# Optimization experiments

Measured on AMD Instinct MI355X. Metric: run time of the kernel, lower is better.

The kernel has to match this reference:

```python
import jax, jax.numpy as jnp
import numpy as np
from jax import lax

B = 16384
NWIRES = 4


def _conv(x, w, b):
    # NCHW conv, stride 1, SAME padding (pad 1 for k=3)
    y = lax.conv_general_dilated(x, w, (1, 1), ((1, 1), (1, 1)),
                                 dimension_numbers=("NCHW", "OIHW", "NCHW"))
    return y + b[None, :, None, None]


def _pool2(x):
    b, c, h, w = x.shape
    return x.reshape(b, c, h // 2, 2, w // 2, 2).max(axis=(3, 5))


def _apply_1q(state, U, wire):
    # state: (B,2,2,2,2) complex; U: (B,2,2) complex
    s = jnp.moveaxis(state, wire + 1, -1)
    s = jnp.einsum("bij,b...j->b...i", U, s)
    return jnp.moveaxis(s, -1, wire + 1)


def _apply_cnot(state, c, t):
    s0 = jnp.take(state, 0, axis=c + 1)
    s1 = jnp.take(state, 1, axis=c + 1)
    ta = t + 1 if t < c else t  # target axis index after removing control axis
    s1 = jnp.flip(s1, axis=ta)
    return jnp.stack([s0, s1], axis=c + 1)


def _ry(th):
    c = jnp.cos(th / 2)
    s = jnp.sin(th / 2)
    U = jnp.stack([jnp.stack([c, -s], -1), jnp.stack([s, c], -1)], -2)
    return U.astype(jnp.complex64)


def _rz(th):
    e = jnp.exp(-0.5j * th.astype(jnp.complex64))
    z = jnp.zeros_like(e)
    return jnp.stack([jnp.stack([e, z], -1), jnp.stack([z, jnp.conj(e)], -1)], -2)


def _rx(th):
    c = jnp.cos(th / 2).astype(jnp.complex64)
    s = jnp.sin(th / 2).astype(jnp.complex64)
    return jnp.stack([jnp.stack([c, -1j * s], -1), jnp.stack([-1j * s, c], -1)], -2)


def _circuit(params):
    # params: (B, 16) -> PauliZ expvals (B, 4)
    b = params.shape[0]
    state = jnp.zeros((b, 16), jnp.complex64).at[:, 0].set(1.0).reshape(b, 2, 2, 2, 2)
    for i in range(NWIRES):
        state = _apply_1q(state, _ry(params[:, 4 * i + 0]), i)
        state = _apply_1q(state, _rz(params[:, 4 * i + 1]), i)
        state = _apply_1q(state, _rx(params[:, 4 * i + 2]), i)
        state = _apply_cnot(state, i, (i + 1) % NWIRES)
    probs = state.real ** 2 + state.imag ** 2  # (B,2,2,2,2)
    zs = []
    for i in range(NWIRES):
        p = probs.sum(axis=tuple(a for a in range(1, 5) if a != i + 1))  # (B,2)
        zs.append(p[:, 0] - p[:, 1])
    return jnp.stack(zs, axis=-1)


def setup_inputs() -> dict:
    key = jax.random.key(0)
    ks = jax.random.split(key, 12)
    d = {}
    d["x"] = jax.random.normal(ks[0], (B, 1, 28, 28), jnp.float32)
    d["conv1_w"] = jax.random.normal(ks[1], (4, 1, 3, 3), jnp.float32) * 0.3
    d["conv1_b"] = jax.random.normal(ks[2], (4,), jnp.float32) * 0.1
    d["conv2_w"] = jax.random.normal(ks[3], (4, 4, 3, 3), jnp.float32) * 0.15
    d["conv2_b"] = jax.random.normal(ks[4], (4,), jnp.float32) * 0.1
    d["pl_w"] = jax.random.normal(ks[5], (16, 196), jnp.float32) * 0.07
    d["pl_b"] = jax.random.normal(ks[6], (16,), jnp.float32) * 0.05
    d["ro_w"] = jax.random.normal(ks[7], (4, 4), jnp.float32) * 0.5
    d["ro_b"] = jax.random.normal(ks[8], (4,), jnp.float32) * 0.1
    d["bn_w"] = jnp.ones((4,), jnp.float32)
    d["bn_b"] = jnp.zeros((4,), jnp.float32)
    return d


def reference(x, conv1_w, conv1_b, conv2_w, conv2_b, pl_w, pl_b, ro_w, ro_b, bn_w, bn_b):
    h = _pool2(jax.nn.relu(_conv(x, conv1_w, conv1_b)))   # (B,4,14,14)
    h = _pool2(jax.nn.relu(_conv(h, conv2_w, conv2_b)))   # (B,4,7,7)
    flat = h.reshape(x.shape[0], -1)                      # (B,196)
    params = flat @ pl_w.T + pl_b                         # (B,16)
    z = _circuit(params)                                  # (B,4)
    out = z @ ro_w.T + ro_b                               # (B,4)
    mean = out.mean(0)
    var = out.var(0)  # biased, matches torch BN training normalization
    return (out - mean) / jnp.sqrt(var + 1e-5) * bn_w + bn_b
```

## Files before the change

kernel.cpp:

```cpp
#include <hip/hip_runtime.h>
#include <math.h>

#define BATCH 16384

__global__ __launch_bounds__(256) void qnat_fused(
    const float* __restrict__ x,
    const float* __restrict__ w1,
    const float* __restrict__ b1,
    const float* __restrict__ w2,
    const float* __restrict__ b2,
    const float* __restrict__ plw,
    const float* __restrict__ plb,
    const float* __restrict__ rw,
    const float* __restrict__ rb,
    float* __restrict__ pre,
    float* __restrict__ stats)
{
  __shared__ float s_w2[144];
  __shared__ __align__(16) float h1p[4][1296];
  __shared__ float h2[4][196];
  __shared__ float s_red[4][8];

  const int tid = threadIdx.x;
  const int w = tid >> 6;
  const int lane = tid & 63;
  const int sample = blockIdx.x * 4 + w;

  if (tid < 144) s_w2[tid] = w2[tid];

  {
    float4 z4 = make_float4(0.f, 0.f, 0.f, 0.f);
    float4* hz = (float4*)&h1p[w][0];
    #pragma unroll
    for (int t = 0; t < 6; t++) {
      int p = t * 64 + lane;
      if (p < 324) hz[p] = z4;
    }
  }
  __syncthreads();

  if (lane < 56) {
    const int i = lane >> 2;
    const int q = lane & 3;
    const float* xb = x + (size_t)sample * 784;
    float win[4][10];
    #pragma unroll
    for (int r = 0; r < 4; r++) {
      int row = 2 * i - 1 + r;
      #pragma unroll
      for (int k = 0; k < 10; k++) win[r][k] = 0.0f;
      if (0 <= row && row < 28) {
        const float* rp = xb + row * 28;
        if (q > 0) win[r][0] = rp[8 * q - 1];
        float4 a = *(const float4*)(rp + 8 * q);
        win[r][1] = a.x; win[r][2] = a.y; win[r][3] = a.z; win[r][4] = a.w;
        if (q < 3) {
          float4 bb = *(const float4*)(rp + 8 * q + 4);
          win[r][5] = bb.x; win[r][6] = bb.y; win[r][7] = bb.z; win[r][8] = bb.w;
          win[r][9] = rp[8 * q + 8];
        }
      }
    }
    float* hb = &h1p[w][20 * (i + 1) + 4 + 4 * q];
    #pragma unroll
    for (int c = 0; c < 4; c++) {
      const float bias = b1[c];
      float m[4];
      #pragma unroll
      for (int jj = 0; jj < 4; jj++) {
        float best = 0.0f;
        #pragma unroll
        for (int py = 0; py < 2; py++)
          #pragma unroll
          for (int px = 0; px < 2; px++) {
            float a = bias;
            #pragma unroll
            for (int dy = 0; dy < 3; dy++)
              #pragma unroll
              for (int dx = 0; dx < 3; dx++)
                a = fmaf(win[py + dy][2 * jj + px + dx], w1[c * 9 + dy * 3 + dx], a);
            best = fmaxf(best, a);
          }
        m[jj] = best;
      }
      if (q < 3) *(float4*)(hb + 320 * c) = make_float4(m[0], m[1], m[2], m[3]);
      else       *(float2*)(hb + 320 * c) = make_float2(m[0], m[1]);
    }
  }

  if (lane < 56) {
    const int co = lane & 3;
    const int jh = (lane >> 2) & 1;
    const int i2 = lane >> 3;
    float acc[4][2][2];
    const float bias2 = b2[co];
    #pragma unroll
    for (int jj = 0; jj < 4; jj++)
      #pragma unroll
      for (int py = 0; py < 2; py++)
        #pragma unroll
        for (int px = 0; px < 2; px++) acc[jj][py][px] = bias2;
    #pragma unroll
    for (int ci = 0; ci < 4; ci++) {
      float win[4][12];
      #pragma unroll
      for (int r = 0; r < 4; r++) {
        const float2* rp = (const float2*)&h1p[w][320 * ci + 20 * (2 * i2 + r) + 2 + 8 * jh];
        #pragma unroll
        for (int t = 0; t < 6; t++) {
          float2 v = rp[t];
          win[r][2 * t] = v.x; win[r][2 * t + 1] = v.y;
        }
      }
      float wv[9];
      #pragma unroll
      for (int t = 0; t < 9; t++) wv[t] = s_w2[(co * 4 + ci) * 9 + t];
      #pragma unroll
      for (int jj = 0; jj < 4; jj++)
        #pragma unroll
        for (int py = 0; py < 2; py++)
          #pragma unroll
          for (int px = 0; px < 2; px++) {
            float a = acc[jj][py][px];
            #pragma unroll
            for (int dy = 0; dy < 3; dy++)
              #pragma unroll
              for (int dx = 0; dx < 3; dx++)
                a = fmaf(win[py + dy][2 * jj + 1 + px + dx], wv[dy * 3 + dx], a);
            acc[jj][py][px] = a;
          }
    }
    #pragma unroll
    for (int jj = 0; jj < 4; jj++) {
      int J = 4 * jh + jj;
      if (J < 7) {
        float m = fmaxf(fmaxf(acc[jj][0][0], acc[jj][0][1]),
                        fmaxf(acc[jj][1][0], acc[jj][1][1]));
        h2[w][49 * co + 7 * i2 + J] = fmaxf(m, 0.0f);
      }
    }
  }

  float cv = 0.0f, sv = 0.0f;
  {
    const int k = lane & 15;
    const int part = lane >> 4;
    const float* hh = &h2[w][part * 49];
    const float* wp = plw + k * 196 + part * 49;
    float s = 0.0f;
    #pragma unroll
    for (int f = 0; f < 49; f++) s = fmaf(hh[f], wp[f], s);
    s += __shfl_down(s, 32, 64);
    s += __shfl_down(s, 16, 64);
    if (lane < 16) {
      float pv = s + plb[k];
      __sincosf(pv * 0.5f, &sv, &cv);
    }
  }

  if (lane < 16) {
    const int l = lane;
    float re = (l == 0) ? 1.0f : 0.0f;
    float im = 0.0f;
    #pragma unroll
    for (int qi = 0; qi < 4; qi++) {
      const int beta = 3 - qi;
      const int m = 1 << beta;
      const int b = (l >> beta) & 1;
      float c = __shfl(cv, 4 * qi, 64), s = __shfl(sv, 4 * qi, 64);
      float pr_ = __shfl_xor(re, m, 64), pi_ = __shfl_xor(im, m, 64);
      float sg = b ? s : -s;
      re = fmaf(c, re, sg * pr_);
      im = fmaf(c, im, sg * pi_);
      c = __shfl(cv, 4 * qi + 1, 64); s = __shfl(sv, 4 * qi + 1, 64);
      float sz = b ? s : -s;
      float nr = c * re - sz * im;
      float ni = c * im + sz * re;
      re = nr; im = ni;
      c = __shfl(cv, 4 * qi + 2, 64); s = __shfl(sv, 4 * qi + 2, 64);
      pr_ = __shfl_xor(re, m, 64); pi_ = __shfl_xor(im, m, 64);
      nr = fmaf(c, re, s * pi_);
      ni = fmaf(c, im, -s * pr_);
      re = nr; im = ni;
      const int tm = 1 << (3 - ((qi + 1) & 3));
      float fr = __shfl_xor(re, tm, 64), fi = __shfl_xor(im, tm, 64);
      if (b) { re = fr; im = fi; }
    }
    float pr2 = re * re + im * im;
    float z0 = ((l >> 3) & 1) ? -pr2 : pr2;
    float z1 = ((l >> 2) & 1) ? -pr2 : pr2;
    float z2 = ((l >> 1) & 1) ? -pr2 : pr2;
    float z3 = (l & 1) ? -pr2 : pr2;
    #pragma unroll
    for (int off = 8; off >= 1; off >>= 1) {
      z0 += __shfl_xor(z0, off, 64);
      z1 += __shfl_xor(z1, off, 64);
      z2 += __shfl_xor(z2, off, 64);
      z3 += __shfl_xor(z3, off, 64);
    }
    if (l == 0) {
      float o0 = fmaf(rw[0],  z0, fmaf(rw[1],  z1, fmaf(rw[2],  z2, fmaf(rw[3],  z3, rb[0]))));
      float o1 = fmaf(rw[4],  z0, fmaf(rw[5],  z1, fmaf(rw[6],  z2, fmaf(rw[7],  z3, rb[1]))));
      float o2 = fmaf(rw[8],  z0, fmaf(rw[9],  z1, fmaf(rw[10], z2, fmaf(rw[11], z3, rb[2]))));
      float o3 = fmaf(rw[12], z0, fmaf(rw[13], z1, fmaf(rw[14], z2, fmaf(rw[15], z3, rb[3]))));
      *(float4*)(pre + (size_t)sample * 4) = make_float4(o0, o1, o2, o3);
      s_red[w][0] = o0; s_red[w][4] = o0 * o0;
      s_red[w][1] = o1; s_red[w][5] = o1 * o1;
      s_red[w][2] = o2; s_red[w][6] = o2 * o2;
      s_red[w][3] = o3; s_red[w][7] = o3 * o3;
    }
  }
  __syncthreads();
  if (tid < 8) {
    float v = s_red[0][tid] + s_red[1][tid] + s_red[2][tid] + s_red[3][tid];
    atomicAdd(&stats[tid], v);
  }
}

__global__ __launch_bounds__(256) void qnat_bn(
    float* __restrict__ pre,
    const float* __restrict__ stats,
    const float* __restrict__ bnw,
    const float* __restrict__ bnb)
{
  int idx = blockIdx.x * 256 + threadIdx.x;
  int c = idx & 3;
  float mean = stats[c] * (1.0f / BATCH);
  float ex2 = stats[4 + c] * (1.0f / BATCH);
  float var = ex2 - mean * mean;
  float inv = rsqrtf(var + 1e-5f);
  pre[idx] = (pre[idx] - mean) * inv * bnw[c] + bnb[c];
}

extern "C" void kernel_launch(void* const* d_in, const int* in_sizes, int n_in,
                              void* d_out, int out_size, void* d_ws, size_t ws_size,
                              hipStream_t stream) {
  const float* x   = (const float*)d_in[0];
  const float* w1  = (const float*)d_in[1];
  const float* b1  = (const float*)d_in[2];
  const float* w2  = (const float*)d_in[3];
  const float* b2  = (const float*)d_in[4];
  const float* plw = (const float*)d_in[5];
  const float* plb = (const float*)d_in[6];
  const float* rw  = (const float*)d_in[7];
  const float* rb  = (const float*)d_in[8];
  const float* bnw = (const float*)d_in[9];
  const float* bnb = (const float*)d_in[10];

  float* out   = (float*)d_out;
  float* stats = (float*)d_ws;

  hipMemsetAsync(stats, 0, 8 * sizeof(float), stream);
  qnat_fused<<<BATCH / 4, 256, 0, stream>>>(x, w1, b1, w2, b2, plw, plb, rw, rb, out, stats);
  qnat_bn<<<(BATCH * 4) / 256, 256, 0, stream>>>(out, stats, bnw, bnb);
}
```

Measured before the change: 162.3 us.

## Remap conv2 to one pooled pixel per lane with compact LDS layout

The second convolution is reorganised so each lane computes one pooled output pixel for all four output channels. It reads a 4x4 window per input channel from a tighter 18-wide padded LDS layout and takes conv2 weights straight from global memory with uniform indices. This removes the shared weight copy and the block-wide barrier. The h2 buffer is padded to a 52-float stride so the projection can use float4 LDS loads. The aim is fewer LDS reads per lane and less synchronisation, in exchange for more register pressure and unaligned scalar stores when writing conv1 output.

```diff
diff --git a/kernel.cpp b/kernel.cpp
--- a/kernel.cpp
+++ b/kernel.cpp
@@ -16,9 +16,8 @@
     float* __restrict__ pre,
     float* __restrict__ stats)
 {
-  __shared__ float s_w2[144];
-  __shared__ __align__(16) float h1p[4][1296];
-  __shared__ float h2[4][196];
+  __shared__ __align__(16) float h1p[4][4 * 288 + 16];
+  __shared__ __align__(16) float h2[4][212];
   __shared__ float s_red[4][8];
 
   const int tid = threadIdx.x;
@@ -26,18 +25,15 @@
   const int lane = tid & 63;
   const int sample = blockIdx.x * 4 + w;
 
-  if (tid < 144) s_w2[tid] = w2[tid];
-
   {
     float4 z4 = make_float4(0.f, 0.f, 0.f, 0.f);
     float4* hz = (float4*)&h1p[w][0];
     #pragma unroll
-    for (int t = 0; t < 6; t++) {
+    for (int t = 0; t < 5; t++) {
       int p = t * 64 + lane;
-      if (p < 324) hz[p] = z4;
-    }
-  }
-  __syncthreads();
+      if (p < 292) hz[p] = z4;
+    }
+  }
 
   if (lane < 56) {
     const int i = lane >> 2;
@@ -61,7 +57,7 @@
         }
       }
     }
-    float* hb = &h1p[w][20 * (i + 1) + 4 + 4 * q];
+    float* hb = &h1p[w][18 * (i + 1) + 1 + 4 * q];
     #pragma unroll
     for (int c = 0; c < 4; c++) {
       const float bias = b1[c];
@@ -83,60 +79,53 @@
           }
         m[jj] = best;
       }
-      if (q < 3) *(float4*)(hb + 320 * c) = make_float4(m[0], m[1], m[2], m[3]);
-      else       *(float2*)(hb + 320 * c) = make_float2(m[0], m[1]);
-    }
-  }
-
-  if (lane < 56) {
-    const int co = lane & 3;
-    const int jh = (lane >> 2) & 1;
+      float* p = hb + 288 * c;
+      if (q < 3) {
+        p[0] = m[0];
+        *(float2*)(p + 1) = make_float2(m[1], m[2]);
+        p[3] = m[3];
+      } else {
+        p[0] = m[0];
+        p[1] = m[1];
+      }
+    }
+  }
+
+  {
+    const int jq = lane & 7;
     const int i2 = lane >> 3;
-    float acc[4][2][2];
-    const float bias2 = b2[co];
-    #pragma unroll
-    for (int jj = 0; jj < 4; jj++)
-      #pragma unroll
-      for (int py = 0; py < 2; py++)
+    if (i2 < 7 && jq < 7) {
+      float win[4][4][4];
+      #pragma unroll
+      for (int ci = 0; ci < 4; ci++) {
+        const float* rp = &h1p[w][288 * ci + 18 * (2 * i2) + 2 * jq];
         #pragma unroll
-        for (int px = 0; px < 2; px++) acc[jj][py][px] = bias2;
-    #pragma unroll
-    for (int ci = 0; ci < 4; ci++) {
-      float win[4][12];
-      #pragma unroll
-      for (int r = 0; r < 4; r++) {
-        const float2* rp = (const float2*)&h1p[w][320 * ci + 20 * (2 * i2 + r) + 2 + 8 * jh];
+        for (int r = 0; r < 4; r++) {
+          float2 a = *(const float2*)(rp + 18 * r);
+          float2 b = *(const float2*)(rp + 18 * r + 2);
+          win[ci][r][0] = a.x; win[ci][r][1] = a.y;
+          win[ci][r][2] = b.x; win[ci][r][3] = b.y;
+        }
+      }
+      #pragma unroll
+      for (int co = 0; co < 4; co++) {
+        const float bias = b2[co];
+        float a00 = bias, a01 = bias, a10 = bias, a11 = bias;
         #pragma unroll
-        for (int t = 0; t < 6; t++) {
-          float2 v = rp[t];
-          win[r][2 * t] = v.x; win[r][2 * t + 1] = v.y;
+        for (int ci = 0; ci < 4; ci++) {
+          #pragma unroll
+          for (int dy = 0; dy < 3; dy++)
+            #pragma unroll
+            for (int dx = 0; dx < 3; dx++) {
+              const float ww = w2[(co * 4 + ci) * 9 + dy * 3 + dx];
+              a00 = fmaf(win[ci][dy][dx],         ww, a00);
+              a01 = fmaf(win[ci][dy][dx + 1],     ww, a01);
+              a10 = fmaf(win[ci][dy + 1][dx],     ww, a10);
+              a11 = fmaf(win[ci][dy + 1][dx + 1], ww, a11);
+            }
         }
-      }
-      float wv[9];
-      #pragma unroll
-      for (int t = 0; t < 9; t++) wv[t] = s_w2[(co * 4 + ci) * 9 + t];
-      #pragma unroll
-      for (int jj = 0; jj < 4; jj++)
-        #pragma unroll
-        for (int py = 0; py < 2; py++)
-          #pragma unroll
-          for (int px = 0; px < 2; px++) {
-            float a = acc[jj][py][px];
-            #pragma unroll
-            for (int dy = 0; dy < 3; dy++)
-              #pragma unroll
-              for (int dx = 0; dx < 3; dx++)
-                a = fmaf(win[py + dy][2 * jj + 1 + px + dx], wv[dy * 3 + dx], a);
-            acc[jj][py][px] = a;
-          }
-    }
-    #pragma unroll
-    for (int jj = 0; jj < 4; jj++) {
-      int J = 4 * jh + jj;
-      if (J < 7) {
-        float m = fmaxf(fmaxf(acc[jj][0][0], acc[jj][0][1]),
-                        fmaxf(acc[jj][1][0], acc[jj][1][1]));
-        h2[w][49 * co + 7 * i2 + J] = fmaxf(m, 0.0f);
+        float m = fmaxf(fmaxf(a00, a01), fmaxf(a10, a11));
+        h2[w][52 * co + 7 * i2 + jq] = fmaxf(m, 0.0f);
       }
     }
   }
@@ -145,11 +134,18 @@
   {
     const int k = lane & 15;
     const int part = lane >> 4;
-    const float* hh = &h2[w][part * 49];
+    const float* hh = &h2[w][52 * part];
     const float* wp = plw + k * 196 + part * 49;
     float s = 0.0f;
     #pragma unroll
-    for (int f = 0; f < 49; f++) s = fmaf(hh[f], wp[f], s);
+    for (int t = 0; t < 12; t++) {
+      float4 hv = *(const float4*)(hh + 4 * t);
+      s = fmaf(hv.x, wp[4 * t + 0], s);
+      s = fmaf(hv.y, wp[4 * t + 1], s);
+      s = fmaf(hv.z, wp[4 * t + 2], s);
+      s = fmaf(hv.w, wp[4 * t + 3], s);
+    }
+    s = fmaf(hh[48], wp[48], s);
     s += __shfl_down(s, 32, 64);
     s += __shfl_down(s, 16, 64);
     if (lane < 16) {
```

Result: faster. 157.0 us (-3.3%).
